# Optimization experiments

Measured on AMD Instinct MI355X. Metric: run time of the kernel, lower is better.

Reference implementation:

```python
import math
import jax, jax.numpy as jnp
import numpy as np

H, PQ, PV, E, C, S, N = 12, 4, 8, 16, 128, 384, 512


def setup_inputs() -> dict:
    key = jax.random.key(0)
    ks = jax.random.split(key, 16)
    rn = lambda k, shape, scale=1.0: jax.random.normal(k, shape, jnp.float32) * scale
    single = rn(ks[0], (N, S))
    pair = rn(ks[1], (N, N, C))
    R, _ = jnp.linalg.qr(rn(ks[2], (N, 3, 3)))  # proper orthonormal frames
    t = rn(ks[3], (N, 3))
    w = 0.02
    return dict(
        single_representation=single,
        pair_representation=pair,
        rotations=R,
        translations=t,
        Wq=rn(ks[4], (H, S, E), w),
        Wk=rn(ks[5], (H, S, E), w),
        Wv=rn(ks[6], (H, S, E), w),
        Wqp=rn(ks[7], (H, PQ, S, 3), w),
        Wkp=rn(ks[8], (H, PQ, S, 3), w),
        Wvp=rn(ks[9], (H, PV, S, 3), w),
        Wb=rn(ks[10], (H, C), w),
        Wout=rn(ks[11], (H * (C + E + PV * 4), S), w),
        b_out=jnp.zeros((S,), jnp.float32),
        scale_head=jnp.ones((H,), jnp.float32),
    )


def _frame_apply(R, t, pts):
    # R:[N,3,3], t:[N,3], pts:[H,P,N,3] -> R_n @ p + t_n per residue n
    return jnp.einsum('nij,hpnj->hpni', R, pts) + t[None, None, :, :]


def reference(single_representation, pair_representation, rotations, translations,
              Wq, Wk, Wv, Wqp, Wkp, Wvp, Wb, Wout, b_out, scale_head):
    single, pair = single_representation, pair_representation
    n = single.shape[0]

    # --- sequence QK term ---
    q = jnp.einsum('nd,hde->hne', single, Wq)
    k = jnp.einsum('nd,hde->hne', single, Wk)
    w_single = math.sqrt(1.0 / E) * jnp.einsum('hne,hme->hnm', q, k)  # [H,N,N]

    # --- pair bias term ---
    w_pair = jnp.einsum('nmc,hc->hnm', pair, Wb)  # [H,N,N]

    # --- frame (3D point distance) term ---
    qp = jnp.einsum('nd,hpdk->hpnk', single, Wqp)  # [H,PQ,N,3]
    kp = jnp.einsum('nd,hpdk->hpnk', single, Wkp)
    lqp = _frame_apply(rotations, translations, qp)
    lkp = _frame_apply(rotations, translations, kp)
    diff = lqp[:, :, :, None, :] - lkp[:, :, None, :, :]   # [H,PQ,N,N,3]
    sqd = jnp.sum(diff * diff, axis=(1, 4))                 # [H,N,N] (sum over points & xyz)
    w_frame = (-math.sqrt(1.0 / (18 * PQ))) * jax.nn.softplus(scale_head)[:, None, None] * sqd

    w = jax.nn.softmax(w_single + w_pair + w_frame, axis=-1)  # [H,N,N]

    # --- sequence value aggregation ---
    v = jnp.einsum('nd,hde->hne', single, Wv)
    att_single = jnp.einsum('hnm,hme->hne', w, v)             # [H,N,E]
    att_single = jnp.transpose(att_single, (1, 0, 2)).reshape(n, -1)

    # --- pair value aggregation (faithful to source: sums over query index too) ---
    colsum = jnp.sum(w, axis=1)                               # [H,N] = sum_a w[h,a,b]
    att_pair = jnp.einsum('hb,ibc->hic', colsum, pair)        # [H,N,C]
    att_pair = jnp.transpose(att_pair, (1, 0, 2)).reshape(n, -1)

    # --- 3D point value aggregation ---
    vp = jnp.einsum('nd,hpdk->hpnk', single, Wvp)             # [H,PV,N,3]
    lvp = _frame_apply(rotations, translations, vp)
    local_out = jnp.einsum('hnm,hpmk->hpnk', w, lvp)          # [H,PV,N,3]
    Rinv = jnp.swapaxes(rotations, -1, -2)                    # R^T
    tinv = -jnp.einsum('nij,nj->ni', Rinv, translations)      # -R^T t
    global_out = _frame_apply(Rinv, tinv, local_out)          # [H,PV,N,3]
    out_points = jnp.transpose(global_out, (2, 1, 0, 3)).reshape(n, -1)  # [N, PV*H*3]
    out_norm = jnp.linalg.norm(global_out, axis=-1)           # [H,PV,N]
    out_norm = jnp.transpose(out_norm, (2, 1, 0)).reshape(n, -1)         # [N, PV*H]

    att = jnp.concatenate([att_single, att_pair, out_points, out_norm], axis=-1)
    return att @ Wout + b_out
```

## Files before the change

### kernel.cpp

```cpp
#include <hip/hip_runtime.h>
#include <math.h>

#define NRES 512
#define HH 12
#define PQn 4
#define PVn 8
#define En 16
#define Cn 128
#define Sn 384
#define ATT_COLS 2112

#define OFF_Q    0
#define OFF_K    (OFF_Q   + HH*NRES*En)
#define OFF_V    (OFF_K   + HH*NRES*En)
#define OFF_LQP  (OFF_V   + HH*NRES*En)
#define OFF_LKP  (OFF_LQP + HH*NRES*12)
#define OFF_LVP  (OFF_LKP + HH*NRES*12)
#define OFF_CS   (OFF_LVP + HH*NRES*24)
#define OFF_ATT  (OFF_CS  + NRES*HH)
#define OFF_LG   (OFF_ATT + NRES*ATT_COLS)
#define OFF_PART OFF_LG
#define KSPLIT 16
#define KCHUNK (ATT_COLS/KSPLIT)
#define OROWS 8

__global__ __launch_bounds__(256) void ipa_proj(
    const float* __restrict__ single, const float* __restrict__ Rm,
    const float* __restrict__ tr,
    const float* __restrict__ Wq, const float* __restrict__ Wk,
    const float* __restrict__ Wv, const float* __restrict__ Wqp,
    const float* __restrict__ Wkp, const float* __restrict__ Wvp,
    float* __restrict__ ws)
{
  float* q   = ws + OFF_Q;  float* k   = ws + OFF_K;  float* v   = ws + OFF_V;
  float* lqp = ws + OFF_LQP; float* lkp = ws + OFF_LKP; float* lvp = ws + OFF_LVP;
  const int n0 = blockIdx.x * 8;
  const int g  = blockIdx.y;
  const int tid = threadIdx.x;
  __shared__ float sS[8][388];
  __shared__ float sR[8][9];
  __shared__ float sT[8][3];
  #pragma unroll
  for (int i = 0; i < 3; ++i) {
    int idx = i*256 + tid;
    int r = idx / 96, c4 = idx % 96;
    float4 val = *reinterpret_cast<const float4*>(single + (size_t)(n0 + r)*Sn + c4*4);
    *reinterpret_cast<float4*>(&sS[r][c4*4]) = val;
  }
  if (tid < 72)      sR[tid/9][tid%9] = Rm[(size_t)(n0 + tid/9)*9 + tid%9];
  else if (tid < 96) { int r = (tid-72)/3; sT[r][(tid-72)%3] = tr[(size_t)(n0+r)*3 + (tid-72)%3]; }
  __syncthreads();
  #pragma unroll
  for (int i = 0; i < 3; ++i) {
    int item = i*256 + tid;
    int nl = item & 7;
    int ul = item >> 3;
    int u  = g*96 + ul;
    const float* srow = sS[nl];
    if (u < 576) {
      int which = u/192, r = u%192, h = r>>4, e = r&15;
      const float* W = (which==0 ? Wq : which==1 ? Wk : Wv) + (size_t)h*Sn*En + e;
      float acc = 0.f;
      #pragma unroll 8
      for (int d = 0; d < Sn; ++d) acc = fmaf(srow[d], W[(size_t)d*En], acc);
      float* dst = (which==0 ? q : which==1 ? k : v);
      dst[((size_t)h*NRES + (n0+nl))*En + e] = acc;
    } else {
      int u2 = u - 576;
      const float* W; float* dst;
      if (u2 < 48)      { int h=u2>>2,     p=u2&3;      W = Wqp + (size_t)(h*PQn+p)*Sn*3; dst = lqp + ((size_t)h*NRES + (n0+nl))*12 + p*3; }
      else if (u2 < 96) { int h=(u2-48)>>2,p=(u2-48)&3; W = Wkp + (size_t)(h*PQn+p)*Sn*3; dst = lkp + ((size_t)h*NRES + (n0+nl))*12 + p*3; }
      else              { int h=(u2-96)>>3,p=(u2-96)&7; W = Wvp + (size_t)(h*PVn+p)*Sn*3; dst = lvp + ((size_t)h*NRES + (n0+nl))*24 + p*3; }
      float x0=0.f,x1=0.f,x2=0.f;
      #pragma unroll 4
      for (int d = 0; d < Sn; ++d) {
        float sv = srow[d];
        x0 = fmaf(sv, W[d*3+0], x0);
        x1 = fmaf(sv, W[d*3+1], x1);
        x2 = fmaf(sv, W[d*3+2], x2);
      }
      const float* R8 = sR[nl]; const float* T8 = sT[nl];
      dst[0] = R8[0]*x0 + R8[1]*x1 + R8[2]*x2 + T8[0];
      dst[1] = R8[3]*x0 + R8[4]*x1 + R8[5]*x2 + T8[1];
      dst[2] = R8[6]*x0 + R8[7]*x1 + R8[8]*x2 + T8[2];
    }
  }
}

__global__ __launch_bounds__(256) void ipa_logits(
    const float* __restrict__ pair, const float* __restrict__ Wb,
    const float* __restrict__ scale_head, float* __restrict__ ws)
{
  const float* q   = ws + OFF_Q;  const float* k   = ws + OFF_K;
  const float* lqp = ws + OFF_LQP; const float* lkp = ws + OFF_LKP;
  float* lg = ws + OFF_LG;
  const int n    = blockIdx.x;
  const int lane = threadIdx.x & 63;
  const int wave = threadIdx.x >> 6;
  const int r    = lane >> 2;
  const int cq   = lane & 3;
  const int m    = blockIdx.y*64 + wave*16 + r;

  const float* prow = pair + ((size_t)n*NRES + m)*Cn;
  float acc[HH];
  #pragma unroll
  for (int h = 0; h < HH; ++h) acc[h] = 0.f;

  #pragma unroll
  for (int jg = 0; jg < 8; ++jg) {
    const int c4 = jg*4 + cq;
    float4 pv = *reinterpret_cast<const float4*>(prow + c4*4);
    const float* wbb = Wb + c4*4;
    #pragma unroll
    for (int h = 0; h < HH; ++h) {
      float4 wb = *reinterpret_cast<const float4*>(wbb + h*Cn);
      acc[h] = fmaf(pv.x, wb.x, acc[h]);
      acc[h] = fmaf(pv.y, wb.y, acc[h]);
      acc[h] = fmaf(pv.z, wb.z, acc[h]);
      acc[h] = fmaf(pv.w, wb.w, acc[h]);
    }
  }
  #pragma unroll
  for (int h = 0; h < HH; ++h) {
    acc[h] += __shfl_xor(acc[h], 1);
    acc[h] += __shfl_xor(acc[h], 2);
  }
  float a0, a1, a2;
  if      (cq == 0) { a0 = acc[0]; a1 = acc[1];  a2 = acc[2];  }
  else if (cq == 1) { a0 = acc[3]; a1 = acc[4];  a2 = acc[5];  }
  else if (cq == 2) { a0 = acc[6]; a1 = acc[7];  a2 = acc[8];  }
  else              { a0 = acc[9]; a1 = acc[10]; a2 = acc[11]; }
  float pb[3] = {a0, a1, a2};

  #pragma unroll
  for (int i = 0; i < 3; ++i) {
    const int h = 3*cq + i;
    const float* qh = q + ((size_t)h*NRES + n)*En;
    const float* kh = k + ((size_t)h*NRES + m)*En;
    float qk = 0.f;
    #pragma unroll
    for (int e = 0; e < En; ++e) qk = fmaf(qh[e], kh[e], qk);
    const float* lq = lqp + ((size_t)h*NRES + n)*12;
    const float* lk = lkp + ((size_t)h*NRES + m)*12;
    float cross = 0.f, Bm = 0.f, An = 0.f;
    #pragma unroll
    for (int jj = 0; jj < 12; ++jj) {
      float a = lq[jj], b = lk[jj];
      cross = fmaf(a, b, cross); Bm = fmaf(b, b, Bm); An = fmaf(a, a, An);
    }
    float gamma = 0.11785113019775793f * __logf(1.f + __expf(scale_head[h]));
    lg[((size_t)h*NRES + n)*NRES + m] = pb[i] + 0.25f*qk - gamma*(An + Bm - 2.f*cross);
  }
}

__global__ __launch_bounds__(256) void ipa_softmax(float* __restrict__ ws)
{
  float* lg = ws + OFF_LG;
  const int row  = blockIdx.x*4 + (threadIdx.x >> 6);
  const int lane = threadIdx.x & 63;
  float4* p = reinterpret_cast<float4*>(lg + (size_t)row*NRES);
  float4 x0 = p[lane];
  float4 x1 = p[64 + lane];
  float mx = fmaxf(fmaxf(fmaxf(x0.x,x0.y),fmaxf(x0.z,x0.w)),
                   fmaxf(fmaxf(x1.x,x1.y),fmaxf(x1.z,x1.w)));
  #pragma unroll
  for (int off = 32; off >= 1; off >>= 1) mx = fmaxf(mx, __shfl_xor(mx, off));
  x0.x = __expf(x0.x-mx); x0.y = __expf(x0.y-mx); x0.z = __expf(x0.z-mx); x0.w = __expf(x0.w-mx);
  x1.x = __expf(x1.x-mx); x1.y = __expf(x1.y-mx); x1.z = __expf(x1.z-mx); x1.w = __expf(x1.w-mx);
  float sum = x0.x+x0.y+x0.z+x0.w + x1.x+x1.y+x1.z+x1.w;
  #pragma unroll
  for (int off = 32; off >= 1; off >>= 1) sum += __shfl_xor(sum, off);
  const float inv = 1.f/sum;
  x0.x*=inv; x0.y*=inv; x0.z*=inv; x0.w*=inv;
  x1.x*=inv; x1.y*=inv; x1.z*=inv; x1.w*=inv;
  p[lane] = x0;
  p[64 + lane] = x1;
}

__global__ __launch_bounds__(256) void ipa_colsum(float* __restrict__ ws)
{
  const float* lg = ws + OFF_LG;
  float* cs = ws + OFF_CS;
  const int h = blockIdx.x, ac = blockIdx.y, tid = threadIdx.x;
  const float* base = lg + (size_t)h*NRES*NRES + (size_t)ac*64*NRES;
  float acc0 = 0.f, acc1 = 0.f;
  #pragma unroll 4
  for (int a = 0; a < 64; ++a) {
    acc0 += base[(size_t)a*NRES + tid];
    acc1 += base[(size_t)a*NRES + tid + 256];
  }
  atomicAdd(&cs[h*NRES + tid],       acc0);
  atomicAdd(&cs[h*NRES + tid + 256], acc1);
}

__global__ __launch_bounds__(256) void ipa_agg(
    const float* __restrict__ Rm, const float* __restrict__ tr,
    float* __restrict__ ws)
{
  const float* v   = ws + OFF_V;
  const float* lvp = ws + OFF_LVP;
  const float* lg  = ws + OFF_LG;
  float* att = ws + OFF_ATT;
  const int row  = blockIdx.x*4 + (threadIdx.x >> 6);
  const int lane = threadIdx.x & 63;
  const int h = row >> 9, n = row & 511;

  float acc[40];
  #pragma unroll
  for (int i = 0; i < 40; ++i) acc[i] = 0.f;

  const float* wrow = lg + (size_t)row*NRES;
  #pragma unroll 2
  for (int j = 0; j < 8; ++j) {
    const int m = j*64 + lane;
    const float wv = wrow[m];
    const float4* v4 = reinterpret_cast<const float4*>(v + ((size_t)h*NRES + m)*En);
    float4 a0=v4[0], a1=v4[1], a2=v4[2], a3=v4[3];
    acc[0]+=wv*a0.x; acc[1]+=wv*a0.y; acc[2]+=wv*a0.z; acc[3]+=wv*a0.w;
    acc[4]+=wv*a1.x; acc[5]+=wv*a1.y; acc[6]+=wv*a1.z; acc[7]+=wv*a1.w;
    acc[8]+=wv*a2.x; acc[9]+=wv*a2.y; acc[10]+=wv*a2.z; acc[11]+=wv*a2.w;
    acc[12]+=wv*a3.x; acc[13]+=wv*a3.y; acc[14]+=wv*a3.z; acc[15]+=wv*a3.w;
    const float4* l4 = reinterpret_cast<const float4*>(lvp + ((size_t)h*NRES + m)*24);
    #pragma unroll
    for (int t = 0; t < 6; ++t) {
      float4 b = l4[t];
      acc[16+4*t+0]+=wv*b.x; acc[16+4*t+1]+=wv*b.y;
      acc[16+4*t+2]+=wv*b.z; acc[16+4*t+3]+=wv*b.w;
    }
  }
  #pragma unroll
  for (int off = 32; off >= 1; off >>= 1) {
    #pragma unroll
    for (int i = 0; i < 40; ++i) acc[i] += __shfl_xor(acc[i], off);
  }
  if (lane == 0) {
    size_t ab = (size_t)n*ATT_COLS;
    float4* as = reinterpret_cast<float4*>(att + ab + h*En);
    as[0] = make_float4(acc[0],acc[1],acc[2],acc[3]);
    as[1] = make_float4(acc[4],acc[5],acc[6],acc[7]);
    as[2] = make_float4(acc[8],acc[9],acc[10],acc[11]);
    as[3] = make_float4(acc[12],acc[13],acc[14],acc[15]);
    const float R0=Rm[n*9+0],R1=Rm[n*9+1],R2=Rm[n*9+2],
                R3=Rm[n*9+3],R4=Rm[n*9+4],R5=Rm[n*9+5],
                R6=Rm[n*9+6],R7=Rm[n*9+7],R8=Rm[n*9+8];
    const float t0=tr[n*3+0], t1=tr[n*3+1], t2=tr[n*3+2];
    #pragma unroll
    for (int pp = 0; pp < 8; ++pp) {
      float d0 = acc[16+3*pp+0]-t0, d1 = acc[16+3*pp+1]-t1, d2 = acc[16+3*pp+2]-t2;
      float g0 = R0*d0 + R3*d1 + R6*d2;
      float g1 = R1*d0 + R4*d1 + R7*d2;
      float g2 = R2*d0 + R5*d1 + R8*d2;
      att[ab + 1728 + (pp*HH + h)*3 + 0] = g0;
      att[ab + 1728 + (pp*HH + h)*3 + 1] = g1;
      att[ab + 1728 + (pp*HH + h)*3 + 2] = g2;
      att[ab + 2016 + pp*HH + h] = sqrtf(g0*g0 + g1*g1 + g2*g2);
    }
  }
}

__global__ __launch_bounds__(256) void ipa_pairagg(
    const float* __restrict__ pair, float* __restrict__ ws)
{
  const float* cs = ws + OFF_CS;
  float* att = ws + OFF_ATT;
  const int i = blockIdx.x, tid = threadIdx.x;
  __shared__ float sCS[HH*NRES];
  __shared__ float4 sRed[8][HH][32];
  #pragma unroll
  for (int it = 0; it < 6; ++it) {
    int idx = it*256 + tid;
    reinterpret_cast<float4*>(sCS)[idx] = reinterpret_cast<const float4*>(cs)[idx];
  }
  __syncthreads();
  const int c4 = tid & 31, bg = tid >> 5;
  float4 acc[HH];
  #pragma unroll
  for (int h = 0; h < HH; ++h) acc[h] = make_float4(0.f,0.f,0.f,0.f);
  const float* prow = pair + (size_t)i*NRES*Cn;
  for (int b = bg; b < NRES; b += 8) {
    float4 pv = *reinterpret_cast<const float4*>(prow + (size_t)b*Cn + c4*4);
    #pragma unroll
    for (int h = 0; h < HH; ++h) {
      float w = sCS[h*NRES + b];
      acc[h].x = fmaf(w, pv.x, acc[h].x);
      acc[h].y = fmaf(w, pv.y, acc[h].y);
      acc[h].z = fmaf(w, pv.z, acc[h].z);
      acc[h].w = fmaf(w, pv.w, acc[h].w);
    }
  }
  #pragma unroll
  for (int h = 0; h < HH; ++h) sRed[bg][h][c4] = acc[h];
  __syncthreads();
  for (int s = 4; s >= 1; s >>= 1) {
    if (bg < s) {
      #pragma unroll
      for (int h = 0; h < HH; ++h) {
        float4 a = sRed[bg][h][c4], b2 = sRed[bg+s][h][c4];
        a.x+=b2.x; a.y+=b2.y; a.z+=b2.z; a.w+=b2.w;
        sRed[bg][h][c4] = a;
      }
    }
    __syncthreads();
  }
  if (bg == 0) {
    size_t base = (size_t)i*ATT_COLS + 192;
    #pragma unroll
    for (int h = 0; h < HH; ++h)
      *reinterpret_cast<float4*>(att + base + h*Cn + c4*4) = sRed[0][h][c4];
  }
}

__global__ __launch_bounds__(384) void ipa_outp(
    const float* __restrict__ att, const float* __restrict__ Wout,
    float* __restrict__ ws)
{
  float* partial = ws + OFF_PART;
  const int rb = blockIdx.x;
  const int ks = blockIdx.y;
  const int s  = threadIdx.x;
  const int n0 = rb*OROWS;
  const int j0 = ks*KCHUNK;

  float acc[OROWS];
  #pragma unroll
  for (int r = 0; r < OROWS; ++r) acc[r] = 0.f;

  for (int jg = 0; jg < KCHUNK/4; ++jg) {
    const int j = j0 + jg*4;
    float w0 = Wout[(size_t)(j+0)*Sn + s];
    float w1 = Wout[(size_t)(j+1)*Sn + s];
    float w2 = Wout[(size_t)(j+2)*Sn + s];
    float w3 = Wout[(size_t)(j+3)*Sn + s];
    #pragma unroll
    for (int r = 0; r < OROWS; ++r) {
      float4 av = *reinterpret_cast<const float4*>(att + (size_t)(n0+r)*ATT_COLS + j);
      acc[r] = fmaf(av.x, w0, acc[r]);
      acc[r] = fmaf(av.y, w1, acc[r]);
      acc[r] = fmaf(av.z, w2, acc[r]);
      acc[r] = fmaf(av.w, w3, acc[r]);
    }
  }
  #pragma unroll
  for (int r = 0; r < OROWS; ++r)
    partial[((size_t)ks*NRES + n0 + r)*Sn + s] = acc[r];
}

__global__ __launch_bounds__(384) void ipa_outred(
    const float* __restrict__ b_out, float* __restrict__ ws,
    float* __restrict__ out)
{
  const float* partial = ws + OFF_PART;
  const int n = blockIdx.x, s = threadIdx.x;
  float a = b_out[s];
  #pragma unroll
  for (int ks = 0; ks < KSPLIT; ++ks)
    a += partial[((size_t)ks*NRES + n)*Sn + s];
  out[(size_t)n*Sn + s] = a;
}

extern "C" void kernel_launch(void* const* d_in, const int* in_sizes, int n_in,
                              void* d_out, int out_size, void* d_ws, size_t ws_size,
                              hipStream_t stream) {
  const float* single = (const float*)d_in[0];
  const float* pair   = (const float*)d_in[1];
  const float* Rm     = (const float*)d_in[2];
  const float* tr     = (const float*)d_in[3];
  const float* Wq     = (const float*)d_in[4];
  const float* Wk     = (const float*)d_in[5];
  const float* Wv     = (const float*)d_in[6];
  const float* Wqp    = (const float*)d_in[7];
  const float* Wkp    = (const float*)d_in[8];
  const float* Wvp    = (const float*)d_in[9];
  const float* Wb     = (const float*)d_in[10];
  const float* Wout   = (const float*)d_in[11];
  const float* b_out  = (const float*)d_in[12];
  const float* scale_head = (const float*)d_in[13];
  float* ws  = (float*)d_ws;
  float* out = (float*)d_out;

  hipMemsetAsync(ws + OFF_CS, 0, NRES*HH*sizeof(float), stream);
  ipa_proj   <<<dim3(64, 8),  256, 0, stream>>>(single, Rm, tr, Wq, Wk, Wv, Wqp, Wkp, Wvp, ws);
  ipa_logits <<<dim3(NRES, 8),256, 0, stream>>>(pair, Wb, scale_head, ws);
  ipa_softmax<<<dim3(HH*NRES/4), 256, 0, stream>>>(ws);
  ipa_colsum <<<dim3(HH, 8),  256, 0, stream>>>(ws);
  ipa_agg    <<<dim3(HH*NRES/4), 256, 0, stream>>>(Rm, tr, ws);
  ipa_pairagg<<<dim3(NRES),   256, 0, stream>>>(pair, ws);
  ipa_outp   <<<dim3(NRES/OROWS, KSPLIT), 384, 0, stream>>>(ws + OFF_ATT, Wout, ws);
  ipa_outred <<<dim3(NRES),   384, 0, stream>>>(b_out, ws, out);
}
```

Before: 314.4 us.

## Precompute packed key terms and restructure logits to one residue per thread

```diff
diff --git a/kernel.cpp b/kernel.cpp
--- a/kernel.cpp
+++ b/kernel.cpp
@@ -20,9 +20,13 @@
 #define OFF_ATT  (OFF_CS  + NRES*HH)
 #define OFF_LG   (OFF_ATT + NRES*ATT_COLS)
 #define OFF_PART OFF_LG
+#define OFF_KC   OFF_ATT
+#define OFF_D1   (OFF_KC + NRES*HH*28)
+#define OFF_D0   (OFF_D1 + NRES*HH)
 #define KSPLIT 16
 #define KCHUNK (ATT_COLS/KSPLIT)
 #define OROWS 8
+#define NGRP 2
 
 __global__ __launch_bounds__(256) void ipa_proj(
     const float* __restrict__ single, const float* __restrict__ Rm,
@@ -87,69 +91,99 @@
   }
 }
 
+__global__ __launch_bounds__(256) void ipa_pack(
+    const float* __restrict__ scale_head, float* __restrict__ ws)
+{
+  const float* k   = ws + OFF_K;
+  const float* lkp = ws + OFF_LKP;
+  const float* lqp = ws + OFF_LQP;
+  float* kc = ws + OFF_KC;
+  float* d1 = ws + OFF_D1;
+  float* d0 = ws + OFF_D0;
+  const int idx = blockIdx.x*256 + threadIdx.x;
+  const int h = idx >> 9, m = idx & 511;
+  const float gamma = 0.11785113019775793f * log1pf(__expf(scale_head[h]));
+  const float* kr  = k   + ((size_t)h*NRES + m)*En;
+  const float* lkr = lkp + ((size_t)h*NRES + m)*12;
+  const float* lqr = lqp + ((size_t)h*NRES + m)*12;
+  float* kcr = kc + ((size_t)m*HH + h)*28;
+  #pragma unroll
+  for (int e = 0; e < En; ++e) kcr[e] = 0.25f * kr[e];
+  float Bm = 0.f, An = 0.f;
+  #pragma unroll
+  for (int j = 0; j < 12; ++j) {
+    float b = lkr[j];
+    kcr[16+j] = (2.f*gamma)*b;
+    Bm = fmaf(b, b, Bm);
+    float a = lqr[j];
+    An = fmaf(a, a, An);
+  }
+  d1[m*HH + h] = -gamma*Bm;
+  d0[m*HH + h] = -gamma*An;
+}
+
 __global__ __launch_bounds__(256) void ipa_logits(
     const float* __restrict__ pair, const float* __restrict__ Wb,
-    const float* __restrict__ scale_head, float* __restrict__ ws)
-{
-  const float* q   = ws + OFF_Q;  const float* k   = ws + OFF_K;
-  const float* lqp = ws + OFF_LQP; const float* lkp = ws + OFF_LKP;
+    float* __restrict__ ws)
+{
+  const float* q   = ws + OFF_Q;
+  const float* lqp = ws + OFF_LQP;
+  const float* kc  = ws + OFF_KC;
+  const float* d1  = ws + OFF_D1;
+  const float* d0  = ws + OFF_D0;
   float* lg = ws + OFF_LG;
-  const int n    = blockIdx.x;
-  const int lane = threadIdx.x & 63;
-  const int wave = threadIdx.x >> 6;
-  const int r    = lane >> 2;
-  const int cq   = lane & 3;
-  const int m    = blockIdx.y*64 + wave*16 + r;
-
-  const float* prow = pair + ((size_t)n*NRES + m)*Cn;
-  float acc[HH];
-  #pragma unroll
-  for (int h = 0; h < HH; ++h) acc[h] = 0.f;
-
-  #pragma unroll
-  for (int jg = 0; jg < 8; ++jg) {
-    const int c4 = jg*4 + cq;
-    float4 pv = *reinterpret_cast<const float4*>(prow + c4*4);
-    const float* wbb = Wb + c4*4;
+  const int n0 = blockIdx.x * NGRP;
+  const int m  = blockIdx.y * 256 + threadIdx.x;
+
+  float acc[NGRP][HH];
+  #pragma unroll
+  for (int g = 0; g < NGRP; ++g)
+    #pragma unroll
+    for (int h = 0; h < HH; ++h) acc[g][h] = 0.f;
+
+  const float4* prow0 = reinterpret_cast<const float4*>(pair + ((size_t)(n0+0)*NRES + m)*Cn);
+  const float4* prow1 = reinterpret_cast<const float4*>(pair + ((size_t)(n0+1)*NRES + m)*Cn);
+  #pragma unroll 4
+  for (int c4 = 0; c4 < 32; ++c4) {
+    float4 p0 = prow0[c4];
+    float4 p1 = prow1[c4];
     #pragma unroll
     for (int h = 0; h < HH; ++h) {
-      float4 wb = *reinterpret_cast<const float4*>(wbb + h*Cn);
-      acc[h] = fmaf(pv.x, wb.x, acc[h]);
-      acc[h] = fmaf(pv.y, wb.y, acc[h]);
-      acc[h] = fmaf(pv.z, wb.z, acc[h]);
-      acc[h] = fmaf(pv.w, wb.w, acc[h]);
-    }
-  }
+      float4 wb = *reinterpret_cast<const float4*>(Wb + h*Cn + c4*4);
+      acc[0][h] += p0.x*wb.x + p0.y*wb.y + p0.z*wb.z + p0.w*wb.w;
+      acc[1][h] += p1.x*wb.x + p1.y*wb.y + p1.z*wb.z + p1.w*wb.w;
+    }
+  }
+
+  float d1v[HH];
+  {
+    const float4* dd = reinterpret_cast<const float4*>(d1 + (size_t)m*HH);
+    float4 a = dd[0], b = dd[1], c = dd[2];
+    d1v[0]=a.x; d1v[1]=a.y; d1v[2]=a.z; d1v[3]=a.w;
+    d1v[4]=b.x; d1v[5]=b.y; d1v[6]=b.z; d1v[7]=b.w;
+    d1v[8]=c.x; d1v[9]=c.y; d1v[10]=c.z; d1v[11]=c.w;
+  }
+
+  const float* kcrow = kc + (size_t)m*HH*28;
   #pragma unroll
   for (int h = 0; h < HH; ++h) {
-    acc[h] += __shfl_xor(acc[h], 1);
-    acc[h] += __shfl_xor(acc[h], 2);
-  }
-  float a0, a1, a2;
-  if      (cq == 0) { a0 = acc[0]; a1 = acc[1];  a2 = acc[2];  }
-  else if (cq == 1) { a0 = acc[3]; a1 = acc[4];  a2 = acc[5];  }
-  else if (cq == 2) { a0 = acc[6]; a1 = acc[7];  a2 = acc[8];  }
-  else              { a0 = acc[9]; a1 = acc[10]; a2 = acc[11]; }
-  float pb[3] = {a0, a1, a2};
-
-  #pragma unroll
-  for (int i = 0; i < 3; ++i) {
-    const int h = 3*cq + i;
-    const float* qh = q + ((size_t)h*NRES + n)*En;
-    const float* kh = k + ((size_t)h*NRES + m)*En;
-    float qk = 0.f;
-    #pragma unroll
-    for (int e = 0; e < En; ++e) qk = fmaf(qh[e], kh[e], qk);
-    const float* lq = lqp + ((size_t)h*NRES + n)*12;
-    const float* lk = lkp + ((size_t)h*NRES + m)*12;
-    float cross = 0.f, Bm = 0.f, An = 0.f;
-    #pragma unroll
-    for (int jj = 0; jj < 12; ++jj) {
-      float a = lq[jj], b = lk[jj];
-      cross = fmaf(a, b, cross); Bm = fmaf(b, b, Bm); An = fmaf(a, a, An);
-    }
-    float gamma = 0.11785113019775793f * __logf(1.f + __expf(scale_head[h]));
-    lg[((size_t)h*NRES + n)*NRES + m] = pb[i] + 0.25f*qk - gamma*(An + Bm - 2.f*cross);
+    const float4* kcr = reinterpret_cast<const float4*>(kcrow + h*28);
+    float4 k0=kcr[0], k1=kcr[1], k2=kcr[2], k3=kcr[3], k4=kcr[4], k5=kcr[5], k6=kcr[6];
+    #pragma unroll
+    for (int g = 0; g < NGRP; ++g) {
+      const int n = n0 + g;
+      const float* qh  = q   + ((size_t)h*NRES + n)*En;
+      const float* lqh = lqp + ((size_t)h*NRES + n)*12;
+      float s = acc[g][h] + d1v[h] + d0[(size_t)n*HH + h];
+      s += k0.x*qh[0]  + k0.y*qh[1]  + k0.z*qh[2]  + k0.w*qh[3];
+      s += k1.x*qh[4]  + k1.y*qh[5]  + k1.z*qh[6]  + k1.w*qh[7];
+      s += k2.x*qh[8]  + k2.y*qh[9]  + k2.z*qh[10] + k2.w*qh[11];
+      s += k3.x*qh[12] + k3.y*qh[13] + k3.z*qh[14] + k3.w*qh[15];
+      s += k4.x*lqh[0] + k4.y*lqh[1] + k4.z*lqh[2] + k4.w*lqh[3];
+      s += k5.x*lqh[4] + k5.y*lqh[5] + k5.z*lqh[6] + k5.w*lqh[7];
+      s += k6.x*lqh[8] + k6.y*lqh[9] + k6.z*lqh[10]+ k6.w*lqh[11];
+      lg[((size_t)h*NRES + n)*NRES + m] = s;
+    }
   }
 }
 
@@ -380,7 +414,8 @@
 
   hipMemsetAsync(ws + OFF_CS, 0, NRES*HH*sizeof(float), stream);
   ipa_proj   <<<dim3(64, 8),  256, 0, stream>>>(single, Rm, tr, Wq, Wk, Wv, Wqp, Wkp, Wvp, ws);
-  ipa_logits <<<dim3(NRES, 8),256, 0, stream>>>(pair, Wb, scale_head, ws);
+  ipa_pack   <<<dim3(24),     256, 0, stream>>>(scale_head, ws);
+  ipa_logits <<<dim3(NRES/NGRP, NRES/256), 256, 0, stream>>>(pair, Wb, ws);
   ipa_softmax<<<dim3(HH*NRES/4), 256, 0, stream>>>(ws);
   ipa_colsum <<<dim3(HH, 8),  256, 0, stream>>>(ws);
   ipa_agg    <<<dim3(HH*NRES/4), 256, 0, stream>>>(Rm, tr, ws);
```

Result: faster. 265.3 us (-15.6%).
